# Performance work log

Measured on AMD Instinct MI355X. Metric: run time of the kernel, lower is better.

## Reference

```python
import jax, jax.numpy as jnp
import numpy as np

B, S, D, H = 4, 2048, 1024, 4
DH = D // H  # per-head dim (dK=dQ=dV)


def setup_inputs() -> dict:
    key = jax.random.key(0)
    ks = jax.random.split(key, 9)
    w = 0.02
    return {
        "q": jax.random.normal(ks[0], (B, S, D), jnp.float32),
        "k": jax.random.normal(ks[1], (B, S, D), jnp.float32),
        "v": jax.random.normal(ks[2], (B, S, D), jnp.float32),
        # shared value projection: Linear(D -> DH)
        "vW": jax.random.normal(ks[3], (DH, D), jnp.float32) * w,
        "vb": jnp.zeros((DH,), jnp.float32),
        # per-head q/k projections stacked over heads: [H, DH, D]
        "qW": jax.random.normal(ks[4], (H, DH, D), jnp.float32) * w,
        "qb": jnp.zeros((H, DH), jnp.float32),
        "kW": jax.random.normal(ks[5], (H, DH, D), jnp.float32) * w,
        "kb": jnp.zeros((H, DH), jnp.float32),
        # output projection wH: Linear(DH -> D, bias=False)
        "wH": jax.random.normal(ks[6], (D, DH), jnp.float32) * w,
    }


def reference(q, k, v, vW, vb, qW, qb, kW, kb, wH):
    # shared V projection: [B,T,DH]
    vs = jnp.einsum("btd,ed->bte", v, vW) + vb
    # batched per-head Q/K projections: [B,H,S,DH]
    qs = jnp.einsum("bsd,hed->bhse", q, qW) + qb[None, :, None, :]
    ks_ = jnp.einsum("btd,hed->bhte", k, kW) + kb[None, :, None, :]
    # scaled dot-product attention (scale by sqrt(dK)), softmax over keys
    scale = jnp.sqrt(jnp.asarray(DH, qs.dtype))
    attn = jnp.einsum("bhse,bhte->bhst", qs, ks_) / scale  # [B,H,S,T]
    attn = jax.nn.softmax(attn, axis=-1)
    # attention applied to shared V: [B,H,S,DH]
    head = jnp.einsum("bhst,bte->bhse", attn, vs)
    # mean over heads, then wH projection (no bias)
    out = jnp.einsum("bse,fe->bsf", jnp.mean(head, axis=1), wH)  # [B,S,D]
    # torch stacks attn at dim=2 -> [B,S,H,T]
    attn_out = jnp.transpose(attn, (0, 2, 1, 3))
    return (out, attn_out)
```

## Files before the change

### kernel.cpp

```cpp
#include <hip/hip_runtime.h>
#include <hip/hip_bf16.h>
#include <stdint.h>

#define B_ 4
#define S_ 2048
#define D_ 1024
#define H_ 4
#define DH_ 256

typedef __bf16 bf16x8 __attribute__((ext_vector_type(8)));
typedef float f32x4 __attribute__((ext_vector_type(4)));

#define MFMA16(a, b, c) __builtin_amdgcn_mfma_f32_16x16x32_bf16(a, b, c, 0, 0, 0)

typedef __attribute__((address_space(1))) const unsigned int gu32;
typedef __attribute__((address_space(3))) unsigned int lu32;
#define GLD16(g, l) __builtin_amdgcn_global_load_lds((gu32*)(g), (lu32*)(l), 16, 0, 0)

__device__ __forceinline__ short f2bf(float f) {
    __bf16 h = (__bf16)f;
    return __builtin_bit_cast(short, h);
}

__global__ void cvt_kernel(const float* __restrict__ src, short* __restrict__ dst, int n4) {
    int i = blockIdx.x * blockDim.x + threadIdx.x;
    if (i >= n4) return;
    float4 f = ((const float4*)src)[i];
    short4 o;
    o.x = f2bf(f.x); o.y = f2bf(f.y); o.z = f2bf(f.z); o.w = f2bf(f.w);
    ((short4*)dst)[i] = o;
}

template<int MODE>
__global__ __launch_bounds__(256)
void gemm_bt(const short* __restrict__ A, long sA, int lda,
             const short* __restrict__ Bw, long sB, int ldb,
             const float* __restrict__ bias,
             void* __restrict__ outp, int K) {
    __shared__ short Ash[128 * 64];
    __shared__ short Bsh[128 * 64];
    const int tid = threadIdx.x, wid = tid >> 6, lane = tid & 63;
    const int bz = blockIdx.z;
    const int tile_m = blockIdx.y * 128, tile_n = blockIdx.x * 128;
    const short* Ab = A + (long)bz * sA + (long)tile_m * lda;
    const short* Bb = Bw + (long)bz * sB + (long)tile_n * ldb;
    const int wr = wid >> 1, wc = wid & 1;

    f32x4 acc[4][4];
#pragma unroll
    for (int i = 0; i < 4; i++)
#pragma unroll
        for (int j = 0; j < 4; j++) acc[i][j] = {0.f, 0.f, 0.f, 0.f};

    for (int k0 = 0; k0 < K; k0 += 64) {
        __syncthreads();
#pragma unroll
        for (int i = 0; i < 4; i++) {
            int off = ((i * 4 + wid) * 64 + lane) * 16;
            int row = off >> 7;
            int col = (off & 127) >> 1;
            GLD16(Ab + row * lda + k0 + col, ((char*)Ash) + off);
            GLD16(Bb + row * ldb + k0 + col, ((char*)Bsh) + off);
        }
        __syncthreads();
#pragma unroll
        for (int kk = 0; kk < 2; kk++) {
            bf16x8 af[4], bfr[4];
#pragma unroll
            for (int mi = 0; mi < 4; mi++)
                af[mi] = *(const bf16x8*)&Ash[(wr * 64 + mi * 16 + (lane & 15)) * 64 + kk * 32 + (lane >> 4) * 8];
#pragma unroll
            for (int ni = 0; ni < 4; ni++)
                bfr[ni] = *(const bf16x8*)&Bsh[(wc * 64 + ni * 16 + (lane & 15)) * 64 + kk * 32 + (lane >> 4) * 8];
#pragma unroll
            for (int mi = 0; mi < 4; mi++)
#pragma unroll
                for (int ni = 0; ni < 4; ni++)
                    acc[mi][ni] = MFMA16(af[mi], bfr[ni], acc[mi][ni]);
        }
    }
#pragma unroll
    for (int mi = 0; mi < 4; mi++)
#pragma unroll
        for (int ni = 0; ni < 4; ni++)
#pragma unroll
            for (int j = 0; j < 4; j++) {
                int r = tile_m + wr * 64 + mi * 16 + (lane >> 4) * 4 + j;
                int c = tile_n + wc * 64 + ni * 16 + (lane & 15);
                float v = acc[mi][ni][j];
                if (MODE == 0) {
                    v = (v + bias[c]) * 0.0625f;
                    ((short*)outp)[(((long)bz * H_ + (c >> 8)) * S_ + r) * DH_ + (c & 255)] = f2bf(v);
                } else if (MODE == 1) {
                    v += bias[c];
                    ((short*)outp)[(((long)bz * H_ + (c >> 8)) * S_ + r) * DH_ + (c & 255)] = f2bf(v);
                } else if (MODE == 2) {
                    v += bias[r];
                    ((short*)outp)[((long)bz * DH_ + r) * S_ + c] = f2bf(v);
                } else {
                    ((float*)outp)[((long)bz * S_ + r) * D_ + c] = v;
                }
            }
}

__global__ __launch_bounds__(512)
void attn_logits(const short* __restrict__ qsc, const short* __restrict__ ksc,
                 float* __restrict__ attnp, float* __restrict__ rowm,
                 float* __restrict__ rowsum) {
    __shared__ short Bsh[8 * 128 * 32];
    __shared__ float sm[2][128], ssm[2][128];
    const int tid = threadIdx.x, wid = tid >> 6, lane = tid & 63;
    const int bh = blockIdx.x;
    const int b = bh >> 2, h = bh & 3;
    const int sg = blockIdx.y * 128;
    const int wr = wid >> 1, wc = wid & 1;
    const short* qbase = qsc + (((long)b * H_ + h) * S_ + sg) * DH_;
    const short* kbase = ksc + (((long)b * H_ + h) * S_) * DH_;
    float* attnbase = attnp + ((long)(b * S_ + sg) * H_ + h) * S_;

    bf16x8 qf[2][8];
    short* Ash = Bsh;
    for (int c = 0; c < 4; c++) {
        __syncthreads();
#pragma unroll
        for (int i = 0; i < 2; i++) {
            int off = ((i * 8 + wid) * 64 + lane) * 16;
            int row = off >> 7;
            int col = (off & 127) >> 1;
            GLD16(qbase + row * DH_ + c * 64 + col, ((char*)Ash) + off);
        }
        __syncthreads();
#pragma unroll
        for (int mi = 0; mi < 2; mi++)
#pragma unroll
            for (int cc = 0; cc < 2; cc++)
                qf[mi][c * 2 + cc] =
                    *(const bf16x8*)&Ash[(wr * 32 + mi * 16 + (lane & 15)) * 64 + cc * 32 + (lane >> 4) * 8];
    }

    float mrun[8], srun[8];
#pragma unroll
    for (int i = 0; i < 8; i++) { mrun[i] = -1e30f; srun[i] = 0.f; }

    for (int tc = 0; tc < 16; tc++) {
        __syncthreads();
#pragma unroll
        for (int i = 0; i < 8; i++) {
            int off = ((i * 8 + wid) * 64 + lane) * 16;
            int e = off >> 1;
            int kk = e >> 12, rem = e & 4095;
            int t = rem >> 5, kc = rem & 31;
            GLD16(kbase + (long)(tc * 128 + t) * DH_ + kk * 32 + kc, ((char*)Bsh) + off);
        }
        __syncthreads();
        f32x4 acc[2][4];
#pragma unroll
        for (int mi = 0; mi < 2; mi++)
#pragma unroll
            for (int ni = 0; ni < 4; ni++) acc[mi][ni] = {0.f, 0.f, 0.f, 0.f};
#pragma unroll
        for (int kk = 0; kk < 8; kk++) {
            bf16x8 bfr[4];
#pragma unroll
            for (int ni = 0; ni < 4; ni++)
                bfr[ni] = *(const bf16x8*)&Bsh[kk * 4096 + (wc * 64 + ni * 16 + (lane & 15)) * 32 + (lane >> 4) * 8];
#pragma unroll
            for (int mi = 0; mi < 2; mi++)
#pragma unroll
                for (int ni = 0; ni < 4; ni++)
                    acc[mi][ni] = MFMA16(qf[mi][kk], bfr[ni], acc[mi][ni]);
        }
#pragma unroll
        for (int mi = 0; mi < 2; mi++)
#pragma unroll
            for (int j = 0; j < 4; j++) {
                float tmax = -1e30f;
#pragma unroll
                for (int ni = 0; ni < 4; ni++) tmax = fmaxf(tmax, acc[mi][ni][j]);
#pragma unroll
                for (int m = 1; m < 16; m <<= 1) tmax = fmaxf(tmax, __shfl_xor(tmax, m, 64));
                float mn = fmaxf(mrun[mi * 4 + j], tmax);
                float ps = 0.f;
#pragma unroll
                for (int ni = 0; ni < 4; ni++) ps += __expf(acc[mi][ni][j] - mn);
#pragma unroll
                for (int m = 1; m < 16; m <<= 1) ps += __shfl_xor(ps, m, 64);
                srun[mi * 4 + j] = srun[mi * 4 + j] * __expf(mrun[mi * 4 + j] - mn) + ps;
                mrun[mi * 4 + j] = mn;
            }
#pragma unroll
        for (int mi = 0; mi < 2; mi++)
#pragma unroll
            for (int ni = 0; ni < 4; ni++)
#pragma unroll
                for (int j = 0; j < 4; j++) {
                    int r = wr * 32 + mi * 16 + (lane >> 4) * 4 + j;
                    int t = tc * 128 + wc * 64 + ni * 16 + (lane & 15);
                    attnbase[(long)r * (H_ * S_) + t] = acc[mi][ni][j];
                }
    }
    __syncthreads();
    if ((lane & 15) == 0) {
#pragma unroll
        for (int mi = 0; mi < 2; mi++)
#pragma unroll
            for (int j = 0; j < 4; j++) {
                int r = wr * 32 + mi * 16 + (lane >> 4) * 4 + j;
                sm[wc][r] = mrun[mi * 4 + j];
                ssm[wc][r] = srun[mi * 4 + j];
            }
    }
    __syncthreads();
    if (tid < 128) {
        float m0 = sm[0][tid], m1 = sm[1][tid];
        float mm = fmaxf(m0, m1);
        float sv = ssm[0][tid] * __expf(m0 - mm) + ssm[1][tid] * __expf(m1 - mm);
        long ridx = ((long)b * H_ + h) * S_ + sg + tid;
        rowm[ridx] = mm;
        rowsum[ridx] = sv;
    }
}

__global__ __launch_bounds__(512)
void attn_pv(float* __restrict__ attnp, const short* __restrict__ vsT,
             const float* __restrict__ rowm, const float* __restrict__ rowsum,
             float* __restrict__ headb) {
    __shared__ short Pl[128 * 64];
    __shared__ short Vsh[256 * 64];
    __shared__ float lm[128], li[128];
    const int tid = threadIdx.x, wid = tid >> 6, lane = tid & 63;
    const int bh = blockIdx.x;
    const int b = bh >> 2, h = bh & 3;
    const int sg = blockIdx.y * 128;
    const int wr = wid >> 2, wc = wid & 3;
    float* attnbase = attnp + ((long)(b * S_ + sg) * H_ + h) * S_;
    const short* vbase = vsT + (long)b * DH_ * S_;

    if (tid < 128) {
        long ridx = ((long)b * H_ + h) * S_ + sg + tid;
        lm[tid] = rowm[ridx];
        li[tid] = 1.f / rowsum[ridx];
    }
    __syncthreads();

    f32x4 acc[4][4];
#pragma unroll
    for (int i = 0; i < 4; i++)
#pragma unroll
        for (int j = 0; j < 4; j++) acc[i][j] = {0.f, 0.f, 0.f, 0.f};

    const int prow0 = tid >> 4, pf4 = tid & 15;
    for (int tc = 0; tc < 32; tc++) {
#pragma unroll
        for (int rr = 0; rr < 4; rr++) {
            int prow = prow0 + rr * 32;
            float* gp = attnbase + (long)prow * (H_ * S_) + tc * 64 + pf4 * 4;
            float4 x = *(const float4*)gp;
            float mm = lm[prow], ii = li[prow];
            float4 p;
            p.x = __expf(x.x - mm) * ii;
            p.y = __expf(x.y - mm) * ii;
            p.z = __expf(x.z - mm) * ii;
            p.w = __expf(x.w - mm) * ii;
            *(float4*)gp = p;
            short4 pb;
            pb.x = f2bf(p.x); pb.y = f2bf(p.y); pb.z = f2bf(p.z); pb.w = f2bf(p.w);
            *(short4*)&Pl[prow * 64 + pf4 * 4] = pb;
        }
#pragma unroll
        for (int i = 0; i < 4; i++) {
            int off = ((i * 8 + wid) * 64 + lane) * 16;
            int e = off >> 1;
            int row = e >> 6, kc = e & 63;
            GLD16(vbase + (long)row * S_ + tc * 64 + kc, ((char*)Vsh) + off);
        }
        __syncthreads();
#pragma unroll
        for (int kk = 0; kk < 2; kk++) {
            bf16x8 af[4], bfr[4];
#pragma unroll
            for (int mi = 0; mi < 4; mi++)
                af[mi] = *(const bf16x8*)&Pl[(wr * 64 + mi * 16 + (lane & 15)) * 64 + kk * 32 + (lane >> 4) * 8];
#pragma unroll
            for (int ni = 0; ni < 4; ni++)
                bfr[ni] = *(const bf16x8*)&Vsh[(wc * 64 + ni * 16 + (lane & 15)) * 64 + kk * 32 + (lane >> 4) * 8];
#pragma unroll
            for (int mi = 0; mi < 4; mi++)
#pragma unroll
                for (int ni = 0; ni < 4; ni++)
                    acc[mi][ni] = MFMA16(af[mi], bfr[ni], acc[mi][ni]);
        }
        __syncthreads();
    }
#pragma unroll
    for (int mi = 0; mi < 4; mi++)
#pragma unroll
        for (int ni = 0; ni < 4; ni++)
#pragma unroll
            for (int j = 0; j < 4; j++) {
                int r = wr * 64 + mi * 16 + (lane >> 4) * 4 + j;
                int c = wc * 64 + ni * 16 + (lane & 15);
                headb[(((long)b * H_ + h) * S_ + sg + r) * DH_ + c] = acc[mi][ni][j];
            }
}

__global__ void head_reduce(const float* __restrict__ headb, short* __restrict__ hmean, int n4) {
    int i = blockIdx.x * blockDim.x + threadIdx.x;
    if (i >= n4) return;
    long f = (long)i * 4;
    int e = (int)(f & (DH_ - 1));
    long bs = f >> 8;
    int b = (int)(bs >> 11), s = (int)(bs & (S_ - 1));
    float4 sum = {0.f, 0.f, 0.f, 0.f};
#pragma unroll
    for (int h = 0; h < H_; h++) {
        float4 a = *(const float4*)&headb[(((long)b * H_ + h) * S_ + s) * DH_ + e];
        sum.x += a.x; sum.y += a.y; sum.z += a.z; sum.w += a.w;
    }
    short4 o;
    o.x = f2bf(sum.x * 0.25f); o.y = f2bf(sum.y * 0.25f);
    o.z = f2bf(sum.z * 0.25f); o.w = f2bf(sum.w * 0.25f);
    *(short4*)&hmean[f] = o;
}

extern "C" void kernel_launch(void* const* d_in, const int* in_sizes, int n_in,
                              void* d_out, int out_size, void* d_ws, size_t ws_size,
                              hipStream_t stream) {
    (void)in_sizes; (void)n_in; (void)out_size; (void)ws_size;
    const float* q = (const float*)d_in[0];
    const float* k = (const float*)d_in[1];
    const float* v = (const float*)d_in[2];
    const float* vW = (const float*)d_in[3];
    const float* vb = (const float*)d_in[4];
    const float* qW = (const float*)d_in[5];
    const float* qb = (const float*)d_in[6];
    const float* kW = (const float*)d_in[7];
    const float* kb = (const float*)d_in[8];
    const float* wH = (const float*)d_in[9];

    long off = 0;
    char* base = (char*)d_ws;
    auto alloc = [&](long bytes) {
        char* p = base + off;
        off = (off + bytes + 255) & ~255L;
        return p;
    };
    short* q_bf = (short*)alloc((long)B_ * S_ * D_ * 2);
    short* k_bf = (short*)alloc((long)B_ * S_ * D_ * 2);
    short* v_bf = (short*)alloc((long)B_ * S_ * D_ * 2);
    short* wq_bf = (short*)alloc((long)H_ * DH_ * D_ * 2);
    short* wk_bf = (short*)alloc((long)H_ * DH_ * D_ * 2);
    short* wv_bf = (short*)alloc((long)DH_ * D_ * 2);
    short* wh_bf = (short*)alloc((long)D_ * DH_ * 2);
    short* qsc = (short*)alloc((long)B_ * H_ * S_ * DH_ * 2);
    short* ksc = (short*)alloc((long)B_ * H_ * S_ * DH_ * 2);
    short* vsT = (short*)alloc((long)B_ * DH_ * S_ * 2);
    float* rowm = (float*)alloc((long)B_ * H_ * S_ * 4);
    float* rowsum = (float*)alloc((long)B_ * H_ * S_ * 4);
    float* headb = (float*)q_bf;
    short* hmean = v_bf;

    float* attnp = (float*)d_out + (long)B_ * S_ * D_;

    auto cvtl = [&](const float* s, short* dst, long n) {
        int n4 = (int)(n / 4);
        cvt_kernel<<<(n4 + 255) / 256, 256, 0, stream>>>(s, dst, n4);
    };
    cvtl(q, q_bf, (long)B_ * S_ * D_);
    cvtl(k, k_bf, (long)B_ * S_ * D_);
    cvtl(v, v_bf, (long)B_ * S_ * D_);
    cvtl(qW, wq_bf, (long)H_ * DH_ * D_);
    cvtl(kW, wk_bf, (long)H_ * DH_ * D_);
    cvtl(vW, wv_bf, (long)DH_ * D_);
    cvtl(wH, wh_bf, (long)D_ * DH_);

    gemm_bt<0><<<dim3(D_ / 128, S_ / 128, B_), 256, 0, stream>>>(
        q_bf, (long)S_ * D_, D_, wq_bf, 0L, D_, qb, qsc, D_);
    gemm_bt<1><<<dim3(D_ / 128, S_ / 128, B_), 256, 0, stream>>>(
        k_bf, (long)S_ * D_, D_, wk_bf, 0L, D_, kb, ksc, D_);
    gemm_bt<2><<<dim3(S_ / 128, DH_ / 128, B_), 256, 0, stream>>>(
        wv_bf, 0L, D_, v_bf, (long)S_ * D_, D_, vb, vsT, D_);

    attn_logits<<<dim3(B_ * H_, S_ / 128), 512, 0, stream>>>(qsc, ksc, attnp, rowm, rowsum);
    attn_pv<<<dim3(B_ * H_, S_ / 128), 512, 0, stream>>>(attnp, vsT, rowm, rowsum, headb);

    int n4 = B_ * S_ * DH_ / 4;
    head_reduce<<<(n4 + 255) / 256, 256, 0, stream>>>(headb, hmean, n4);
    gemm_bt<3><<<dim3(D_ / 128, S_ / 128, B_), 256, 0, stream>>>(
        hmean, (long)S_ * DH_, DH_, wh_bf, 0L, DH_, nullptr, (float*)d_out, DH_);
}
```

Before: 762.2 us.

## Split attention over key halves with smaller tiles and swizzled LDS layouts

Both attention kernels now run on 64-row query tiles with 256 threads and split the key dimension into two halves along a new grid z axis. This multiplies the block count and raises occupancy. Partial softmax statistics and partial PV outputs are written per half and merged in attn_pv and head_reduce. K, V and P tiles in LDS use XOR swizzles to avoid bank conflicts, and attn_pv prefetches the next logits tile into registers. The cost is extra workspace traffic for the second partial head buffer and the stat merge, and the workspace buffers are reshuffled so the larger partial buffer fits.

New measurement: 844.5 us. 1.11x slower.

```diff
diff --git a/kernel.cpp b/kernel.cpp
--- a/kernel.cpp
+++ b/kernel.cpp
@@ -7,6 +7,7 @@
 #define D_ 1024
 #define H_ 4
 #define DH_ 256
+#define BHS_ (B_ * H_ * S_)
 
 typedef __bf16 bf16x8 __attribute__((ext_vector_type(8)));
 typedef float f32x4 __attribute__((ext_vector_type(4)));
@@ -65,18 +66,17 @@
         __syncthreads();
 #pragma unroll
         for (int kk = 0; kk < 2; kk++) {
-            bf16x8 af[4], bfr[4];
+            bf16x8 af[4];
 #pragma unroll
             for (int mi = 0; mi < 4; mi++)
                 af[mi] = *(const bf16x8*)&Ash[(wr * 64 + mi * 16 + (lane & 15)) * 64 + kk * 32 + (lane >> 4) * 8];
 #pragma unroll
-            for (int ni = 0; ni < 4; ni++)
-                bfr[ni] = *(const bf16x8*)&Bsh[(wc * 64 + ni * 16 + (lane & 15)) * 64 + kk * 32 + (lane >> 4) * 8];
-#pragma unroll
-            for (int mi = 0; mi < 4; mi++)
-#pragma unroll
-                for (int ni = 0; ni < 4; ni++)
-                    acc[mi][ni] = MFMA16(af[mi], bfr[ni], acc[mi][ni]);
+            for (int ni = 0; ni < 4; ni++) {
+                bf16x8 bfr = *(const bf16x8*)&Bsh[(wc * 64 + ni * 16 + (lane & 15)) * 64 + kk * 32 + (lane >> 4) * 8];
+#pragma unroll
+                for (int mi = 0; mi < 4; mi++)
+                    acc[mi][ni] = MFMA16(af[mi], bfr, acc[mi][ni]);
+            }
         }
     }
 #pragma unroll
@@ -103,145 +103,115 @@
             }
 }
 
-__global__ __launch_bounds__(512)
+__global__ __launch_bounds__(256, 4)
 void attn_logits(const short* __restrict__ qsc, const short* __restrict__ ksc,
-                 float* __restrict__ attnp, float* __restrict__ rowm,
-                 float* __restrict__ rowsum) {
-    __shared__ short Bsh[8 * 128 * 32];
-    __shared__ float sm[2][128], ssm[2][128];
+                 float* __restrict__ attnp, float* __restrict__ rowm_p,
+                 float* __restrict__ rowsum_p) {
+    __shared__ short Ksh[8 * 64 * 32];
     const int tid = threadIdx.x, wid = tid >> 6, lane = tid & 63;
     const int bh = blockIdx.x;
     const int b = bh >> 2, h = bh & 3;
-    const int sg = blockIdx.y * 128;
-    const int wr = wid >> 1, wc = wid & 1;
+    const int sg = blockIdx.y * 64;
+    const int tz = blockIdx.z;
     const short* qbase = qsc + (((long)b * H_ + h) * S_ + sg) * DH_;
-    const short* kbase = ksc + (((long)b * H_ + h) * S_) * DH_;
-    float* attnbase = attnp + ((long)(b * S_ + sg) * H_ + h) * S_;
-
-    bf16x8 qf[2][8];
-    short* Ash = Bsh;
-    for (int c = 0; c < 4; c++) {
-        __syncthreads();
-#pragma unroll
-        for (int i = 0; i < 2; i++) {
-            int off = ((i * 8 + wid) * 64 + lane) * 16;
-            int row = off >> 7;
-            int col = (off & 127) >> 1;
-            GLD16(qbase + row * DH_ + c * 64 + col, ((char*)Ash) + off);
-        }
-        __syncthreads();
-#pragma unroll
-        for (int mi = 0; mi < 2; mi++)
-#pragma unroll
-            for (int cc = 0; cc < 2; cc++)
-                qf[mi][c * 2 + cc] =
-                    *(const bf16x8*)&Ash[(wr * 32 + mi * 16 + (lane & 15)) * 64 + cc * 32 + (lane >> 4) * 8];
-    }
-
-    float mrun[8], srun[8];
-#pragma unroll
-    for (int i = 0; i < 8; i++) { mrun[i] = -1e30f; srun[i] = 0.f; }
+    const short* kbase = ksc + (((long)b * H_ + h) * S_ + tz * 1024) * DH_;
+    float* attnbase = attnp + ((long)(b * S_ + sg) * H_ + h) * S_ + tz * 1024;
+
+    bf16x8 qf[8];
+    {
+        const short* qrow = qbase + (wid * 16 + (lane & 15)) * DH_ + (lane >> 4) * 8;
+#pragma unroll
+        for (int kk = 0; kk < 8; kk++) qf[kk] = *(const bf16x8*)(qrow + kk * 32);
+    }
+
+    float mrun[4], srun[4];
+#pragma unroll
+    for (int j = 0; j < 4; j++) { mrun[j] = -1e30f; srun[j] = 0.f; }
 
     for (int tc = 0; tc < 16; tc++) {
         __syncthreads();
 #pragma unroll
         for (int i = 0; i < 8; i++) {
-            int off = ((i * 8 + wid) * 64 + lane) * 16;
-            int e = off >> 1;
-            int kk = e >> 12, rem = e & 4095;
-            int t = rem >> 5, kc = rem & 31;
-            GLD16(kbase + (long)(tc * 128 + t) * DH_ + kk * 32 + kc, ((char*)Bsh) + off);
-        }
-        __syncthreads();
-        f32x4 acc[2][4];
-#pragma unroll
-        for (int mi = 0; mi < 2; mi++)
-#pragma unroll
-            for (int ni = 0; ni < 4; ni++) acc[mi][ni] = {0.f, 0.f, 0.f, 0.f};
+            int off = ((i * 4 + wid) * 64 + lane) * 16;
+            int kk = off >> 12, rem = off & 4095;
+            int t = rem >> 6, kb = rem & 63;
+            int kbs = kb ^ ((((t >> 1) & 3)) << 4);
+            GLD16(kbase + (long)(tc * 64 + t) * DH_ + kk * 32 + (kbs >> 1), ((char*)Ksh) + off);
+        }
+        __syncthreads();
+        f32x4 acc[4];
+#pragma unroll
+        for (int ni = 0; ni < 4; ni++) acc[ni] = {0.f, 0.f, 0.f, 0.f};
 #pragma unroll
         for (int kk = 0; kk < 8; kk++) {
-            bf16x8 bfr[4];
-#pragma unroll
-            for (int ni = 0; ni < 4; ni++)
-                bfr[ni] = *(const bf16x8*)&Bsh[kk * 4096 + (wc * 64 + ni * 16 + (lane & 15)) * 32 + (lane >> 4) * 8];
-#pragma unroll
-            for (int mi = 0; mi < 2; mi++)
-#pragma unroll
-                for (int ni = 0; ni < 4; ni++)
-                    acc[mi][ni] = MFMA16(qf[mi][kk], bfr[ni], acc[mi][ni]);
-        }
-#pragma unroll
-        for (int mi = 0; mi < 2; mi++)
+#pragma unroll
+            for (int ni = 0; ni < 4; ni++) {
+                int t = ni * 16 + (lane & 15);
+                int kbyte = ((lane >> 4) * 16) ^ ((((t >> 1) & 3)) << 4);
+                bf16x8 bfr = *(const bf16x8*)(((const char*)Ksh) + kk * 4096 + t * 64 + kbyte);
+                acc[ni] = MFMA16(qf[kk], bfr, acc[ni]);
+            }
+        }
+#pragma unroll
+        for (int j = 0; j < 4; j++) {
+            float tmax = fmaxf(fmaxf(acc[0][j], acc[1][j]), fmaxf(acc[2][j], acc[3][j]));
+#pragma unroll
+            for (int m = 1; m < 16; m <<= 1) tmax = fmaxf(tmax, __shfl_xor(tmax, m, 64));
+            float mn = fmaxf(mrun[j], tmax);
+            float ps = 0.f;
+#pragma unroll
+            for (int ni = 0; ni < 4; ni++) ps += __expf(acc[ni][j] - mn);
+#pragma unroll
+            for (int m = 1; m < 16; m <<= 1) ps += __shfl_xor(ps, m, 64);
+            srun[j] = srun[j] * __expf(mrun[j] - mn) + ps;
+            mrun[j] = mn;
+        }
+#pragma unroll
+        for (int ni = 0; ni < 4; ni++)
 #pragma unroll
             for (int j = 0; j < 4; j++) {
-                float tmax = -1e30f;
-#pragma unroll
-                for (int ni = 0; ni < 4; ni++) tmax = fmaxf(tmax, acc[mi][ni][j]);
-#pragma unroll
-                for (int m = 1; m < 16; m <<= 1) tmax = fmaxf(tmax, __shfl_xor(tmax, m, 64));
-                float mn = fmaxf(mrun[mi * 4 + j], tmax);
-                float ps = 0.f;
-#pragma unroll
-                for (int ni = 0; ni < 4; ni++) ps += __expf(acc[mi][ni][j] - mn);
-#pragma unroll
-                for (int m = 1; m < 16; m <<= 1) ps += __shfl_xor(ps, m, 64);
-                srun[mi * 4 + j] = srun[mi * 4 + j] * __expf(mrun[mi * 4 + j] - mn) + ps;
-                mrun[mi * 4 + j] = mn;
-            }
-#pragma unroll
-        for (int mi = 0; mi < 2; mi++)
-#pragma unroll
-            for (int ni = 0; ni < 4; ni++)
-#pragma unroll
-                for (int j = 0; j < 4; j++) {
-                    int r = wr * 32 + mi * 16 + (lane >> 4) * 4 + j;
-                    int t = tc * 128 + wc * 64 + ni * 16 + (lane & 15);
-                    attnbase[(long)r * (H_ * S_) + t] = acc[mi][ni][j];
-                }
-    }
-    __syncthreads();
+                int r = wid * 16 + (lane >> 4) * 4 + j;
+                int t = tc * 64 + ni * 16 + (lane & 15);
+                attnbase[(long)r * (H_ * S_) + t] = acc[ni][j];
+            }
+    }
     if ((lane & 15) == 0) {
 #pragma unroll
-        for (int mi = 0; mi < 2; mi++)
-#pragma unroll
-            for (int j = 0; j < 4; j++) {
-                int r = wr * 32 + mi * 16 + (lane >> 4) * 4 + j;
-                sm[wc][r] = mrun[mi * 4 + j];
-                ssm[wc][r] = srun[mi * 4 + j];
-            }
-    }
-    __syncthreads();
-    if (tid < 128) {
-        float m0 = sm[0][tid], m1 = sm[1][tid];
-        float mm = fmaxf(m0, m1);
-        float sv = ssm[0][tid] * __expf(m0 - mm) + ssm[1][tid] * __expf(m1 - mm);
-        long ridx = ((long)b * H_ + h) * S_ + sg + tid;
-        rowm[ridx] = mm;
-        rowsum[ridx] = sv;
-    }
-}
-
-__global__ __launch_bounds__(512)
+        for (int j = 0; j < 4; j++) {
+            int r = wid * 16 + (lane >> 4) * 4 + j;
+            long ridx = (long)tz * BHS_ + ((long)b * H_ + h) * S_ + sg + r;
+            rowm_p[ridx] = mrun[j];
+            rowsum_p[ridx] = srun[j];
+        }
+    }
+}
+
+__global__ __launch_bounds__(256, 4)
 void attn_pv(float* __restrict__ attnp, const short* __restrict__ vsT,
-             const float* __restrict__ rowm, const float* __restrict__ rowsum,
-             float* __restrict__ headb) {
-    __shared__ short Pl[128 * 64];
+             const float* __restrict__ rowm_p, const float* __restrict__ rowsum_p,
+             float* __restrict__ headp) {
+    __shared__ short Pl[64 * 64];
     __shared__ short Vsh[256 * 64];
-    __shared__ float lm[128], li[128];
     const int tid = threadIdx.x, wid = tid >> 6, lane = tid & 63;
     const int bh = blockIdx.x;
     const int b = bh >> 2, h = bh & 3;
-    const int sg = blockIdx.y * 128;
-    const int wr = wid >> 2, wc = wid & 3;
-    float* attnbase = attnp + ((long)(b * S_ + sg) * H_ + h) * S_;
-    const short* vbase = vsT + (long)b * DH_ * S_;
-
-    if (tid < 128) {
-        long ridx = ((long)b * H_ + h) * S_ + sg + tid;
-        lm[tid] = rowm[ridx];
-        li[tid] = 1.f / rowsum[ridx];
-    }
-    __syncthreads();
+    const int sg = blockIdx.y * 64;
+    const int tz = blockIdx.z;
+    float* attnbase = attnp + ((long)(b * S_ + sg) * H_ + h) * S_ + tz * 1024;
+    const short* vbase = vsT + (long)b * DH_ * S_ + tz * 1024;
+
+    const int prow0 = tid >> 4, pcol = (tid & 15) * 4;
+    float lm[4], li[4];
+#pragma unroll
+    for (int rr = 0; rr < 4; rr++) {
+        long ridx = ((long)b * H_ + h) * S_ + sg + prow0 + rr * 16;
+        float m0 = rowm_p[ridx], m1 = rowm_p[BHS_ + ridx];
+        float s0 = rowsum_p[ridx], s1 = rowsum_p[BHS_ + ridx];
+        float mm = fmaxf(m0, m1);
+        float sv = s0 * __expf(m0 - mm) + s1 * __expf(m1 - mm);
+        lm[rr] = mm;
+        li[rr] = 1.f / sv;
+    }
 
     f32x4 acc[4][4];
 #pragma unroll
@@ -249,46 +219,58 @@
 #pragma unroll
         for (int j = 0; j < 4; j++) acc[i][j] = {0.f, 0.f, 0.f, 0.f};
 
-    const int prow0 = tid >> 4, pf4 = tid & 15;
-    for (int tc = 0; tc < 32; tc++) {
+    float4 p[4];
+#pragma unroll
+    for (int rr = 0; rr < 4; rr++)
+        p[rr] = *(const float4*)(attnbase + (long)(prow0 + rr * 16) * (H_ * S_) + pcol);
+
+    for (int tc = 0; tc < 16; tc++) {
+#pragma unroll
+        for (int i = 0; i < 8; i++) {
+            int off = ((i * 4 + wid) * 64 + lane) * 16;
+            int e = off >> 7, cb = off & 127;
+            int cbs = cb ^ ((e & 7) << 4);
+            GLD16(vbase + (long)e * S_ + tc * 64 + (cbs >> 1), ((char*)Vsh) + off);
+        }
 #pragma unroll
         for (int rr = 0; rr < 4; rr++) {
-            int prow = prow0 + rr * 32;
-            float* gp = attnbase + (long)prow * (H_ * S_) + tc * 64 + pf4 * 4;
-            float4 x = *(const float4*)gp;
-            float mm = lm[prow], ii = li[prow];
-            float4 p;
-            p.x = __expf(x.x - mm) * ii;
-            p.y = __expf(x.y - mm) * ii;
-            p.z = __expf(x.z - mm) * ii;
-            p.w = __expf(x.w - mm) * ii;
-            *(float4*)gp = p;
+            int prow = prow0 + rr * 16;
+            float4 x = p[rr];
+            float4 pr;
+            pr.x = __expf(x.x - lm[rr]) * li[rr];
+            pr.y = __expf(x.y - lm[rr]) * li[rr];
+            pr.z = __expf(x.z - lm[rr]) * li[rr];
+            pr.w = __expf(x.w - lm[rr]) * li[rr];
+            *(float4*)(attnbase + (long)prow * (H_ * S_) + tc * 64 + pcol) = pr;
             short4 pb;
-            pb.x = f2bf(p.x); pb.y = f2bf(p.y); pb.z = f2bf(p.z); pb.w = f2bf(p.w);
-            *(short4*)&Pl[prow * 64 + pf4 * 4] = pb;
-        }
-#pragma unroll
-        for (int i = 0; i < 4; i++) {
-            int off = ((i * 8 + wid) * 64 + lane) * 16;
-            int e = off >> 1;
-            int row = e >> 6, kc = e & 63;
-            GLD16(vbase + (long)row * S_ + tc * 64 + kc, ((char*)Vsh) + off);
-        }
-        __syncthreads();
+            pb.x = f2bf(pr.x); pb.y = f2bf(pr.y); pb.z = f2bf(pr.z); pb.w = f2bf(pr.w);
+            int wb = (prow * 128 + pcol * 2) ^ ((prow & 7) << 4);
+            *(short4*)(((char*)Pl) + wb) = pb;
+        }
+        __syncthreads();
+        if (tc < 15) {
+#pragma unroll
+            for (int rr = 0; rr < 4; rr++)
+                p[rr] = *(const float4*)(attnbase + (long)(prow0 + rr * 16) * (H_ * S_) + (tc + 1) * 64 + pcol);
+        }
 #pragma unroll
         for (int kk = 0; kk < 2; kk++) {
-            bf16x8 af[4], bfr[4];
-#pragma unroll
-            for (int mi = 0; mi < 4; mi++)
-                af[mi] = *(const bf16x8*)&Pl[(wr * 64 + mi * 16 + (lane & 15)) * 64 + kk * 32 + (lane >> 4) * 8];
-#pragma unroll
-            for (int ni = 0; ni < 4; ni++)
-                bfr[ni] = *(const bf16x8*)&Vsh[(wc * 64 + ni * 16 + (lane & 15)) * 64 + kk * 32 + (lane >> 4) * 8];
-#pragma unroll
-            for (int mi = 0; mi < 4; mi++)
-#pragma unroll
-                for (int ni = 0; ni < 4; ni++)
-                    acc[mi][ni] = MFMA16(af[mi], bfr[ni], acc[mi][ni]);
+            bf16x8 af[4];
+#pragma unroll
+            for (int mi = 0; mi < 4; mi++) {
+                int s = mi * 16 + (lane & 15);
+                int bo = (s * 128 + kk * 64 + (lane >> 4) * 16) ^ ((s & 7) << 4);
+                af[mi] = *(const bf16x8*)(((const char*)Pl) + bo);
+            }
+#pragma unroll
+            for (int ni = 0; ni < 4; ni++) {
+                int e = wid * 64 + ni * 16 + (lane & 15);
+                int bo = (e * 128 + kk * 64 + (lane >> 4) * 16) ^ ((e & 7) << 4);
+                bf16x8 bfr = *(const bf16x8*)(((const char*)Vsh) + bo);
+#pragma unroll
+                for (int mi = 0; mi < 4; mi++)
+                    acc[mi][ni] = MFMA16(af[mi], bfr, acc[mi][ni]);
+            }
         }
         __syncthreads();
     }
@@ -298,25 +280,29 @@
         for (int ni = 0; ni < 4; ni++)
 #pragma unroll
             for (int j = 0; j < 4; j++) {
-                int r = wr * 64 + mi * 16 + (lane >> 4) * 4 + j;
-                int c = wc * 64 + ni * 16 + (lane & 15);
-                headb[(((long)b * H_ + h) * S_ + sg + r) * DH_ + c] = acc[mi][ni][j];
-            }
-}
-
-__global__ void head_reduce(const float* __restrict__ headb, short* __restrict__ hmean, int n4) {
+                int r = mi * 16 + (lane >> 4) * 4 + j;
+                int c = wid * 64 + ni * 16 + (lane & 15);
+                headp[(long)tz * ((long)B_ * H_ * S_ * DH_) +
+                      (((long)b * H_ + h) * S_ + sg + r) * DH_ + c] = acc[mi][ni][j];
+            }
+}
+
+__global__ void head_reduce(const float* __restrict__ headp, short* __restrict__ hmean, int n4) {
     int i = blockIdx.x * blockDim.x + threadIdx.x;
     if (i >= n4) return;
     long f = (long)i * 4;
     int e = (int)(f & (DH_ - 1));
     long bs = f >> 8;
     int b = (int)(bs >> 11), s = (int)(bs & (S_ - 1));
+    const long BHSD = (long)B_ * H_ * S_ * DH_;
     float4 sum = {0.f, 0.f, 0.f, 0.f};
 #pragma unroll
-    for (int h = 0; h < H_; h++) {
-        float4 a = *(const float4*)&headb[(((long)b * H_ + h) * S_ + s) * DH_ + e];
-        sum.x += a.x; sum.y += a.y; sum.z += a.z; sum.w += a.w;
-    }
+    for (int z = 0; z < 2; z++)
+#pragma unroll
+        for (int h = 0; h < H_; h++) {
+            float4 a = *(const float4*)&headp[z * BHSD + (((long)b * H_ + h) * S_ + s) * DH_ + e];
+            sum.x += a.x; sum.y += a.y; sum.z += a.z; sum.w += a.w;
+        }
     short4 o;
     o.x = f2bf(sum.x * 0.25f); o.y = f2bf(sum.y * 0.25f);
     o.z = f2bf(sum.z * 0.25f); o.w = f2bf(sum.w * 0.25f);
@@ -345,20 +331,20 @@
         off = (off + bytes + 255) & ~255L;
         return p;
     };
+    short* wh_bf = (short*)alloc((long)D_ * DH_ * 2);
     short* q_bf = (short*)alloc((long)B_ * S_ * D_ * 2);
     short* k_bf = (short*)alloc((long)B_ * S_ * D_ * 2);
     short* v_bf = (short*)alloc((long)B_ * S_ * D_ * 2);
     short* wq_bf = (short*)alloc((long)H_ * DH_ * D_ * 2);
     short* wk_bf = (short*)alloc((long)H_ * DH_ * D_ * 2);
     short* wv_bf = (short*)alloc((long)DH_ * D_ * 2);
-    short* wh_bf = (short*)alloc((long)D_ * DH_ * 2);
     short* qsc = (short*)alloc((long)B_ * H_ * S_ * DH_ * 2);
     short* ksc = (short*)alloc((long)B_ * H_ * S_ * DH_ * 2);
     short* vsT = (short*)alloc((long)B_ * DH_ * S_ * 2);
-    float* rowm = (float*)alloc((long)B_ * H_ * S_ * 4);
-    float* rowsum = (float*)alloc((long)B_ * H_ * S_ * 4);
-    float* headb = (float*)q_bf;
-    short* hmean = v_bf;
+    float* rowm_p = (float*)alloc(2L * BHS_ * 4);
+    float* rowsum_p = (float*)alloc(2L * BHS_ * 4);
+    float* headp = (float*)q_bf;
+    short* hmean = ksc;
 
     float* attnp = (float*)d_out + (long)B_ * S_ * D_;
 
@@ -381,11 +367,11 @@
     gemm_bt<2><<<dim3(S_ / 128, DH_ / 128, B_), 256, 0, stream>>>(
         wv_bf, 0L, D_, v_bf, (long)S_ * D_, D_, vb, vsT, D_);
 
-    attn_logits<<<dim3(B_ * H_, S_ / 128), 512, 0, stream>>>(qsc, ksc, attnp, rowm, rowsum);
-    attn_pv<<<dim3(B_ * H_, S_ / 128), 512, 0, stream>>>(attnp, vsT, rowm, rowsum, headb);
+    attn_logits<<<dim3(B_ * H_, S_ / 64, 2), 256, 0, stream>>>(qsc, ksc, attnp, rowm_p, rowsum_p);
+    attn_pv<<<dim3(B_ * H_, S_ / 64, 2), 256, 0, stream>>>(attnp, vsT, rowm_p, rowsum_p, headp);
 
     int n4 = B_ * S_ * DH_ / 4;
-    head_reduce<<<(n4 + 255) / 256, 256, 0, stream>>>(headb, hmean, n4);
+    head_reduce<<<(n4 + 255) / 256, 256, 0, stream>>>(headp, hmean, n4);
     gemm_bt<3><<<dim3(D_ / 128, S_ / 128, B_), 256, 0, stream>>>(
         hmean, (long)S_ * DH_, DH_, wh_bf, 0L, DH_, nullptr, (float*)d_out, DH_);
 }
```
